# Performance work log

Hardware: AMD Instinct MI355X
Metric: run time of the kernel (lower is better)

Reference implementation:

```python
import jax, jax.numpy as jnp
import numpy as np

B, N, D, H, F = 16, 257, 1024, 16, 4096
HD = D // H
EPS = 1e-5
GATING_TEMP = 0.25  # gating_hyperparam for steep_sigmoid
SCALE = HD ** -0.5


def layer_norm(x, g, b):
    mu = jnp.mean(x, axis=-1, keepdims=True)
    var = jnp.mean(jnp.square(x - mu), axis=-1, keepdims=True)
    return (x - mu) * jax.lax.rsqrt(var + EPS) * g + b


def quick_gelu(x):
    return x * jax.nn.sigmoid(1.702 * x)


def setup_inputs() -> dict:
    key = jax.random.key(0)
    ks = jax.random.split(key, 24)
    s = 0.02
    inp = {
        'hidden_states': jax.random.normal(ks[0], (B, N, D), jnp.float32),
        'cached_hidden': jax.random.normal(ks[1], (B, N, D), jnp.float32),
        'cached_q': jax.random.normal(ks[2], (B, N, D), jnp.float32),
        'cached_k': jax.random.normal(ks[3], (B, N, D), jnp.float32),
        'cached_v': jax.random.normal(ks[4], (B, N, D), jnp.float32),
        'ln1_g': jnp.ones((D,), jnp.float32),
        'ln1_b': jnp.zeros((D,), jnp.float32),
        'wq': jax.random.normal(ks[5], (D, D), jnp.float32) * s,
        'bq': jnp.zeros((D,), jnp.float32),
        'wk': jax.random.normal(ks[6], (D, D), jnp.float32) * s,
        'bk': jnp.zeros((D,), jnp.float32),
        'wv': jax.random.normal(ks[7], (D, D), jnp.float32) * s,
        'bv': jnp.zeros((D,), jnp.float32),
        'wo': jax.random.normal(ks[8], (D, D), jnp.float32) * s,
        'bo': jnp.zeros((D,), jnp.float32),
        'ln2_g': jnp.ones((D,), jnp.float32),
        'ln2_b': jnp.zeros((D,), jnp.float32),
        'w1': jax.random.normal(ks[9], (D, F), jnp.float32) * s,
        'b1': jnp.zeros((F,), jnp.float32),
        'w2': jax.random.normal(ks[10], (F, D), jnp.float32) * s,
        'b2': jnp.zeros((D,), jnp.float32),
        'threshold': jnp.float32(0.5),
    }
    return inp


def reference(hidden_states, cached_hidden, cached_q, cached_k, cached_v,
              ln1_g, ln1_b, wq, bq, wk, bk, wv, bv, wo, bo,
              ln2_g, ln2_b, w1, b1, w2, b2, threshold):
    # layer_norm1 + QKV projection (layer_norm1_qkv_projection)
    h_ln = layer_norm(hidden_states, ln1_g, ln1_b)
    q = h_ln @ wq + bq
    k = h_ln @ wk + bk
    v = h_ln @ wv + bv

    # reuse module: cosine^1 similarity vs cached hidden, steep_sigmoid gating
    # against learned threshold; soft gather/scatter blend of cached states.
    num = jnp.sum(cached_hidden * hidden_states, axis=-1)           # [B,N]
    den = (jnp.linalg.norm(cached_hidden, axis=-1)
           * jnp.linalg.norm(hidden_states, axis=-1) + 1e-8)
    sim = num / den                                                 # [B,N]
    gate = jax.nn.sigmoid((sim - threshold) / GATING_TEMP)[..., None]  # [B,N,1]

    hidden = gate * cached_hidden + (1.0 - gate) * hidden_states
    q = gate * cached_q + (1.0 - gate) * q
    k = gate * cached_k + (1.0 - gate) * k
    v = gate * cached_v + (1.0 - gate) * v

    # manual bmm-softmax-bmm attention
    qh = (q * SCALE).reshape(B, N, H, HD).transpose(0, 2, 1, 3)  # [B,H,N,hd]
    kh = k.reshape(B, N, H, HD).transpose(0, 2, 1, 3)
    vh = v.reshape(B, N, H, HD).transpose(0, 2, 1, 3)
    scores = jnp.einsum('bhqd,bhkd->bhqk', qh, kh)
    probs = jax.nn.softmax(scores, axis=-1)
    attn = jnp.einsum('bhqk,bhkd->bhqd', probs, vh)
    attn = attn.transpose(0, 2, 1, 3).reshape(B, N, D)
    attn = attn @ wo + bo

    hidden = hidden + attn
    residual = hidden
    hidden = layer_norm(hidden, ln2_g, ln2_b)
    hidden = quick_gelu(hidden @ w1 + b1) @ w2 + b2
    return residual + hidden
```

## Files before the change

### kernel.cpp

```cpp
#include <hip/hip_runtime.h>
#include <hip/hip_bf16.h>
#include <stdint.h>

#define BB   16
#define SEQ  257
#define DD   1024
#define NH   16
#define HD_  64
#define FF   4096
#define MM   (BB*SEQ)
#define MPAD2 4352
#define SPAD 272
#define VPAD 288
#define SCALE_Q 0.125f

typedef __bf16 bf16x8 __attribute__((ext_vector_type(8)));
typedef float  f32x4  __attribute__((ext_vector_type(4)));
typedef unsigned short u16;

__device__ __forceinline__ u16 f2bf(float f) {
  uint32_t u = __float_as_uint(f);
  uint32_t r = (u + 0x7FFFu + ((u >> 16) & 1u)) >> 16;
  return (u16)r;
}
__device__ __forceinline__ float bf2f(u16 u) {
  return __uint_as_float(((uint32_t)u) << 16);
}
__device__ __forceinline__ void gll16(const void* g, void* l) {
  __builtin_amdgcn_global_load_lds(
      (const __attribute__((address_space(1))) void*)g,
      (__attribute__((address_space(3))) void*)l, 16, 0, 0);
}
__device__ __forceinline__ float wsum(float v) {
  #pragma unroll
  for (int o = 1; o < 64; o <<= 1) v += __shfl_xor(v, o);
  return v;
}

__global__ __launch_bounds__(256) void transpose_kernel(
    const float* __restrict__ in, u16* __restrict__ out, int R, int C) {
  __shared__ float tile[64][65];
  int ctiles = C >> 6;
  int r0 = (blockIdx.x / ctiles) << 6, c0 = (blockIdx.x % ctiles) << 6;
  int tx = threadIdx.x & 63, ty = threadIdx.x >> 6;
  #pragma unroll
  for (int it = 0; it < 16; ++it) {
    int rr = it * 4 + ty;
    tile[rr][tx] = in[(size_t)(r0 + rr) * C + c0 + tx];
  }
  __syncthreads();
  #pragma unroll
  for (int it = 0; it < 16; ++it) {
    int rr = it * 4 + ty;
    out[(size_t)(c0 + rr) * R + r0 + tx] = f2bf(tile[tx][rr]);
  }
}

__global__ __launch_bounds__(256) void vtrans_kernel(
    const u16* __restrict__ vb, u16* __restrict__ vt) {
  __shared__ u16 tile[64][72];
  const int bh = blockIdx.x, c = blockIdx.y;
  const int tx = threadIdx.x & 63, ty = threadIdx.x >> 6;
  const u16* src = vb + (size_t)bh * SPAD * HD_;
  u16* dst = vt + (size_t)bh * HD_ * VPAD;
  #pragma unroll
  for (int it = 0; it < 16; ++it) {
    int r = it * 4 + ty;
    int nn = c * 64 + r;  int nnc = nn < SPAD ? nn : SPAD - 1;
    tile[r][tx] = src[(size_t)nnc * HD_ + tx];
  }
  __syncthreads();
  #pragma unroll
  for (int it = 0; it < 16; ++it) {
    int hd = it * 4 + ty;
    int col = c * 64 + tx;
    if (col < VPAD) dst[(size_t)hd * VPAD + col] = tile[tx][hd];
  }
}

__global__ __launch_bounds__(256) void ln1_gate_kernel(
    const float* __restrict__ h, const float* __restrict__ c,
    const float* __restrict__ g, const float* __restrict__ bta,
    const float* __restrict__ thr, u16* __restrict__ hln,
    float* __restrict__ hblend, float* __restrict__ gate) {
  int m = blockIdx.x, t = threadIdx.x, l = t & 63, w = t >> 6;
  const float4 hv = *(const float4*)(h + (size_t)m * DD + t * 4);
  const float4 cv = *(const float4*)(c + (size_t)m * DD + t * 4);
  float sh = hv.x + hv.y + hv.z + hv.w;
  float sh2 = hv.x*hv.x + hv.y*hv.y + hv.z*hv.z + hv.w*hv.w;
  float sch = hv.x*cv.x + hv.y*cv.y + hv.z*cv.z + hv.w*cv.w;
  float sc2 = cv.x*cv.x + cv.y*cv.y + cv.z*cv.z + cv.w*cv.w;
  sh = wsum(sh); sh2 = wsum(sh2); sch = wsum(sch); sc2 = wsum(sc2);
  __shared__ float red[4][4];
  if (l == 0) { red[w][0]=sh; red[w][1]=sh2; red[w][2]=sch; red[w][3]=sc2; }
  __syncthreads();
  float Sh  = red[0][0]+red[1][0]+red[2][0]+red[3][0];
  float Sh2 = red[0][1]+red[1][1]+red[2][1]+red[3][1];
  float Sch = red[0][2]+red[1][2]+red[2][2]+red[3][2];
  float Sc2 = red[0][3]+red[1][3]+red[2][3]+red[3][3];
  float mean = Sh * (1.f/DD);
  float var  = Sh2 * (1.f/DD) - mean*mean;
  float rs   = rsqrtf(var + 1e-5f);
  float sim  = Sch / (sqrtf(Sc2)*sqrtf(Sh2) + 1e-8f);
  float gv   = 1.f / (1.f + __expf(-(sim - thr[0]) * 4.0f));
  float4 gg = *(const float4*)(g + t*4);
  float4 bb = *(const float4*)(bta + t*4);
  ushort4 ob;
  ob.x = f2bf((hv.x-mean)*rs*gg.x + bb.x);
  ob.y = f2bf((hv.y-mean)*rs*gg.y + bb.y);
  ob.z = f2bf((hv.z-mean)*rs*gg.z + bb.z);
  ob.w = f2bf((hv.w-mean)*rs*gg.w + bb.w);
  *(ushort4*)(hln + (size_t)m * DD + t * 4) = ob;
  float4 hb;
  hb.x = gv*cv.x + (1.f-gv)*hv.x;  hb.y = gv*cv.y + (1.f-gv)*hv.y;
  hb.z = gv*cv.z + (1.f-gv)*hv.z;  hb.w = gv*cv.w + (1.f-gv)*hv.w;
  *(float4*)(hblend + (size_t)m * DD + t * 4) = hb;
  if (t == 0) gate[m] = gv;
}

__global__ __launch_bounds__(256) void ln2_kernel(
    const float* __restrict__ in, const float* __restrict__ g,
    const float* __restrict__ bta, u16* __restrict__ outb) {
  int m = blockIdx.x, t = threadIdx.x, l = t & 63, w = t >> 6;
  const float4 hv = *(const float4*)(in + (size_t)m * DD + t * 4);
  float sh = hv.x + hv.y + hv.z + hv.w;
  float sh2 = hv.x*hv.x + hv.y*hv.y + hv.z*hv.z + hv.w*hv.w;
  sh = wsum(sh); sh2 = wsum(sh2);
  __shared__ float red[4][2];
  if (l == 0) { red[w][0] = sh; red[w][1] = sh2; }
  __syncthreads();
  float Sh  = red[0][0]+red[1][0]+red[2][0]+red[3][0];
  float Sh2 = red[0][1]+red[1][1]+red[2][1]+red[3][1];
  float mean = Sh * (1.f/DD);
  float rs = rsqrtf(Sh2 * (1.f/DD) - mean*mean + 1e-5f);
  float4 gg = *(const float4*)(g + t*4);
  float4 bb = *(const float4*)(bta + t*4);
  ushort4 ob;
  ob.x = f2bf((hv.x-mean)*rs*gg.x + bb.x);
  ob.y = f2bf((hv.y-mean)*rs*gg.y + bb.y);
  ob.z = f2bf((hv.z-mean)*rs*gg.z + bb.z);
  ob.w = f2bf((hv.w-mean)*rs*gg.w + bb.w);
  *(ushort4*)(outb + (size_t)m * DD + t * 4) = ob;
}

#define VMW4 do { asm volatile("s_waitcnt vmcnt(4)" ::: "memory"); \
                  __builtin_amdgcn_sched_barrier(0); } while(0)
#define VMW0 do { asm volatile("s_waitcnt vmcnt(0)" ::: "memory"); \
                  __builtin_amdgcn_sched_barrier(0); } while(0)

#define STG_A(T_, KS_, SLOT_) do { \
  const u16* _g = pA + (T_)*64 + (KS_)*32; \
  gll16(_g, &sA[SLOT_][KS_][0] + tid*8); \
  gll16(_g + rowStep, &sA[SLOT_][KS_][0] + 4096 + tid*8); } while(0)
#define STG_B(T_, KS_, SLOT_) do { \
  const u16* _g = pB + (T_)*64 + (KS_)*32; \
  gll16(_g, &sB[SLOT_][KS_][0] + tid*8); \
  gll16(_g + rowStep, &sB[SLOT_][KS_][0] + 4096 + tid*8); } while(0)

#define PHASE(SLOT_, KS_, MH_, RB_, STG_STMT, VM_STMT) do { \
  { const u16* _pa = &sA[SLOT_][KS_][aBase + (MH_)*2048]; \
    av[0] = *(const bf16x8*)(_pa);      av[1] = *(const bf16x8*)(_pa+512); \
    av[2] = *(const bf16x8*)(_pa+1024); av[3] = *(const bf16x8*)(_pa+1536); } \
  if (RB_) { const u16* _pb = &sB[SLOT_][KS_][bBase]; \
    fv[0] = *(const bf16x8*)(_pb);      fv[1] = *(const bf16x8*)(_pb+512); \
    fv[2] = *(const bf16x8*)(_pb+1024); fv[3] = *(const bf16x8*)(_pb+1536); } \
  STG_STMT; \
  __builtin_amdgcn_s_barrier(); \
  asm volatile("s_waitcnt lgkmcnt(0)" ::: "memory"); \
  __builtin_amdgcn_sched_barrier(0); \
  __builtin_amdgcn_s_setprio(1); \
  _Pragma("unroll") \
  for (int f = 0; f < 4; ++f) \
    _Pragma("unroll") \
    for (int n = 0; n < 4; ++n) \
      acc[(MH_)*4+f][n] = __builtin_amdgcn_mfma_f32_16x16x32_bf16( \
          av[f], fv[n], acc[(MH_)*4+f][n], 0, 0, 0); \
  __builtin_amdgcn_s_setprio(0); \
  VM_STMT; \
  __builtin_amdgcn_s_barrier(); } while(0)

template<int EPI, int KT>
__global__ __launch_bounds__(512, 2) void gemm256(
    const u16* __restrict__ A, const u16* __restrict__ Bt,
    int Kstride, int kBase0,
    const float* __restrict__ bias,
    const float* __restrict__ gate,
    const float* __restrict__ c0, const float* __restrict__ c1, const float* __restrict__ c2,
    const float* __restrict__ bq, const float* __restrict__ bk, const float* __restrict__ bvp,
    u16* __restrict__ qb, u16* __restrict__ kb, u16* __restrict__ vb,
    u16* __restrict__ outb, u16* __restrict__ partb) {
  const int tid = threadIdx.x, w = tid >> 6, l = tid & 63, lr = l & 15, lh = l >> 4;
  const int wm = w >> 2, wn = w & 3;
  const int n0 = blockIdx.x * 256, m0 = blockIdx.y * 256;
  const int kBase = kBase0 + blockIdx.z * (KT * 64);

  __shared__ u16 sA[2][2][8192];
  __shared__ u16 sB[2][2][8192];

  f32x4 acc[8][4];
  f32x4 zero = {0.f, 0.f, 0.f, 0.f};
  #pragma unroll
  for (int i = 0; i < 8; ++i)
    #pragma unroll
    for (int j = 0; j < 4; ++j) acc[i][j] = zero;

  const int rS = tid >> 2, cS = (tid & 3) * 8;
  const u16* pA = A  + (size_t)(m0 + rS) * Kstride + kBase + cS;
  const u16* pB = Bt + (size_t)(n0 + rS) * Kstride + kBase + cS;
  const size_t rowStep = (size_t)128 * Kstride;

  const int aBase = (wm*128 + lr) * 32 + lh * 8;
  const int bBase = (wn*64  + lr) * 32 + lh * 8;
  bf16x8 av[4], fv[4];

  STG_A(0,0,0);  STG_B(0,0,0);
  STG_A(0,1,0);  STG_B(0,1,0);
  STG_A(1,0,1);  STG_B(1,0,1);
  asm volatile("s_waitcnt vmcnt(4)" ::: "memory");
  __builtin_amdgcn_sched_barrier(0);
  __builtin_amdgcn_s_barrier();

  #pragma unroll 1
  for (int i = 0; i < KT/2 - 1; ++i) {
    const int jB = 2*i+1, nA = 2*i+2, nB = 2*i+3;
    PHASE(0,0,0,1, STG_A(jB,1,1), ((void)0));
    PHASE(0,0,1,0, STG_B(jB,1,1), ((void)0));
    PHASE(0,1,0,1, STG_A(nA,0,0), ((void)0));
    PHASE(0,1,1,0, STG_B(nA,0,0), VMW4);
    PHASE(1,0,0,1, STG_A(nA,1,0), ((void)0));
    PHASE(1,0,1,0, STG_B(nA,1,0), ((void)0));
    PHASE(1,1,0,1, STG_A(nB,0,1), ((void)0));
    PHASE(1,1,1,0, STG_B(nB,0,1), VMW4);
  }
  PHASE(0,0,0,1, STG_A(KT-1,1,1), ((void)0));
  PHASE(0,0,1,0, STG_B(KT-1,1,1), ((void)0));
  PHASE(0,1,0,1, ((void)0), ((void)0));
  PHASE(0,1,1,0, ((void)0), VMW0);
  PHASE(1,0,0,1, ((void)0), ((void)0));
  PHASE(1,0,1,0, ((void)0), ((void)0));
  PHASE(1,1,0,1, ((void)0), ((void)0));
  PHASE(1,1,1,0, ((void)0), ((void)0));

  const int crow = m0 + wm*128, ccol = n0 + wn*64;
  if constexpr (EPI == 0) {
    const int which = n0 >> 10;
    const float* cb = which==0 ? bq : (which==1 ? bk : bvp);
    const float* cp = which==0 ? c0 : (which==1 ? c1 : c2);
    u16* dst = which==0 ? qb : (which==1 ? kb : vb);
    const float scl = which==0 ? SCALE_Q : 1.0f;
    #pragma unroll
    for (int mi = 0; mi < 8; ++mi)
      #pragma unroll
      for (int rr = 0; rr < 4; ++rr) {
        const int row = crow + mi*16 + lh*4 + rr;
        if (row < MM) {
          const float gv = gate[row];
          const int bidx = row / SEQ, nn = row - bidx * SEQ;
          #pragma unroll
          for (int ni = 0; ni < 4; ++ni) {
            const int col = ccol + ni*16 + lr;
            const int d = col & 1023, hd = d & 63, hh = d >> 6;
            const float lin = acc[mi][ni][rr] + cb[d];
            const float val = (gv * cp[(size_t)row*DD + d] + (1.f - gv) * lin) * scl;
            dst[((size_t)(bidx*NH + hh)*SPAD + nn)*HD_ + hd] = f2bf(val);
          }
        }
      }
  } else if constexpr (EPI == 2) {
    #pragma unroll
    for (int mi = 0; mi < 8; ++mi)
      #pragma unroll
      for (int rr = 0; rr < 4; ++rr) {
        const int row = crow + mi*16 + lh*4 + rr;
        if (row < MM) {
          #pragma unroll
          for (int ni = 0; ni < 4; ++ni) {
            const int col = ccol + ni*16 + lr;
            const float x = acc[mi][ni][rr] + bias[col];
            const float s = 1.f / (1.f + __expf(-1.702f * x));
            outb[(size_t)row*FF + col] = f2bf(x * s);
          }
        }
      }
  } else {
    u16* pp = partb + (size_t)blockIdx.z * ((size_t)MPAD2 * 1024);
    #pragma unroll
    for (int mi = 0; mi < 8; ++mi)
      #pragma unroll
      for (int rr = 0; rr < 4; ++rr) {
        const int row = crow + mi*16 + lh*4 + rr;
        if (row < MM) {
          #pragma unroll
          for (int ni = 0; ni < 4; ++ni) {
            const int col = ccol + ni*16 + lr;
            pp[(size_t)row*1024 + col] = f2bf(acc[mi][ni][rr]);
          }
        }
      }
  }
}

__global__ __launch_bounds__(256) void reduce_mlp2(
    const u16* __restrict__ parts, const float* __restrict__ bias,
    const float* __restrict__ resid, float* __restrict__ out) {
  const size_t PS = (size_t)MPAD2 * 1024;
  const int row = blockIdx.x, t = threadIdx.x, c = t * 4;
  const size_t base = (size_t)row * 1024 + c;
  float4 r = *(const float4*)(resid + base);
  float4 b = *(const float4*)(bias + c);
  float o0 = r.x + b.x, o1 = r.y + b.y, o2 = r.z + b.z, o3 = r.w + b.w;
  #pragma unroll
  for (int p = 0; p < 4; ++p) {
    ushort4 u = *(const ushort4*)(parts + p*PS + base);
    o0 += bf2f(u.x);  o1 += bf2f(u.y);  o2 += bf2f(u.z);  o3 += bf2f(u.w);
  }
  float4 o;  o.x = o0;  o.y = o1;  o.z = o2;  o.w = o3;
  *(float4*)(out + base) = o;
}

template<int EPI>
__global__ __launch_bounds__(256) void gemm_bt(
    const u16* __restrict__ A, const u16* __restrict__ Bt, int K,
    const float* __restrict__ bias,
    const float* __restrict__ addsrc, float* __restrict__ outf) {
  const int tid = threadIdx.x, w = tid >> 6, l = tid & 63, lr = l & 15, lh = l >> 4;
  const int n0 = blockIdx.x * 128, m0 = blockIdx.y * 128;
  const int wm = w >> 1, wn = w & 1;
  __shared__ u16 sA[2][4096], sB[2][4096];
  f32x4 acc[4][4];
  f32x4 zero = {0.f, 0.f, 0.f, 0.f};
  #pragma unroll
  for (int i = 0; i < 4; ++i)
    #pragma unroll
    for (int j = 0; j < 4; ++j) acc[i][j] = zero;

  const int r0 = tid >> 2, cc = (tid & 3) * 8;
  const u16* ga0 = A  + (size_t)(m0 + r0) * K + cc;
  const u16* ga1 = A  + (size_t)(m0 + 64 + r0) * K + cc;
  const u16* gb0 = Bt + (size_t)(n0 + r0) * K + cc;
  const u16* gb1 = Bt + (size_t)(n0 + 64 + r0) * K + cc;

  const int nt = K >> 5;
  gll16(ga0, &sA[0][w*512]);  gll16(ga1, &sA[0][2048 + w*512]);
  gll16(gb0, &sB[0][w*512]);  gll16(gb1, &sB[0][2048 + w*512]);

  for (int t = 0; t < nt; ++t) {
    const int cur = t & 1;
    __syncthreads();
    if (t + 1 < nt) {
      const int k0 = (t + 1) << 5;
      gll16(ga0 + k0, &sA[cur^1][w*512]);  gll16(ga1 + k0, &sA[cur^1][2048 + w*512]);
      gll16(gb0 + k0, &sB[cur^1][w*512]);  gll16(gb1 + k0, &sB[cur^1][2048 + w*512]);
    }
    bf16x8 af[4], bfr[4];
    #pragma unroll
    for (int mi = 0; mi < 4; ++mi)
      af[mi] = *(const bf16x8*)&sA[cur][(wm*64 + mi*16 + lr)*32 + lh*8];
    #pragma unroll
    for (int ni = 0; ni < 4; ++ni)
      bfr[ni] = *(const bf16x8*)&sB[cur][(wn*64 + ni*16 + lr)*32 + lh*8];
    #pragma unroll
    for (int mi = 0; mi < 4; ++mi)
      #pragma unroll
      for (int ni = 0; ni < 4; ++ni)
        acc[mi][ni] = __builtin_amdgcn_mfma_f32_16x16x32_bf16(af[mi], bfr[ni], acc[mi][ni], 0, 0, 0);
  }

  #pragma unroll
  for (int mi = 0; mi < 4; ++mi)
    #pragma unroll
    for (int r = 0; r < 4; ++r) {
      const int row = m0 + wm*64 + mi*16 + lh*4 + r;
      if (row < MM) {
        #pragma unroll
        for (int ni = 0; ni < 4; ++ni) {
          const int col = n0 + wn*64 + ni*16 + lr;
          outf[(size_t)row*DD + col] = acc[mi][ni][r] + bias[col] + addsrc[(size_t)row*DD + col];
        }
      }
    }
}

__global__ __launch_bounds__(256) void attn_kernel(
    const u16* __restrict__ qb, const u16* __restrict__ kb,
    const u16* __restrict__ vt, u16* __restrict__ attn_out) {
  __shared__ u16 P[64 * 296];
  const int bh = blockIdx.x, b = bh >> 4, hh = bh & 15;
  const int q0 = blockIdx.y * 64;
  const int tid = threadIdx.x, w = tid >> 6, l = tid & 63, lr = l & 15, lh = l >> 4;
  const u16* qp = qb + (size_t)bh * SPAD * HD_;
  const u16* kp = kb + (size_t)bh * SPAD * HD_;
  const u16* vp = vt + (size_t)bh * HD_ * VPAD;

  const int qr = q0 + w*16 + lr;
  const int qrc = qr < 271 ? qr : 271;
  bf16x8 aq0 = *(const bf16x8*)(qp + (size_t)qrc*HD_ + lh*8);
  bf16x8 aq1 = *(const bf16x8*)(qp + (size_t)qrc*HD_ + 32 + lh*8);

  f32x4 st[18];
  f32x4 zero = {0.f,0.f,0.f,0.f};
  #pragma unroll
  for (int t = 0; t < 18; ++t) st[t] = zero;
  #pragma unroll
  for (int t = 0; t < 18; ++t) {
    int key = t*16 + lr;  int keyc = key < 271 ? key : 271;
    bf16x8 b0 = *(const bf16x8*)(kp + (size_t)keyc*HD_ + lh*8);
    bf16x8 b1 = *(const bf16x8*)(kp + (size_t)keyc*HD_ + 32 + lh*8);
    st[t] = __builtin_amdgcn_mfma_f32_16x16x32_bf16(aq0, b0, st[t], 0, 0, 0);
    st[t] = __builtin_amdgcn_mfma_f32_16x16x32_bf16(aq1, b1, st[t], 0, 0, 0);
  }
  #pragma unroll
  for (int t = 0; t < 18; ++t) {
    int key = t*16 + lr;
    if (key >= SEQ) { st[t][0]=-1e30f; st[t][1]=-1e30f; st[t][2]=-1e30f; st[t][3]=-1e30f; }
  }
  float mr[4], sr[4];
  #pragma unroll
  for (int r = 0; r < 4; ++r) {
    float m = st[0][r];
    #pragma unroll
    for (int t = 1; t < 18; ++t) m = fmaxf(m, st[t][r]);
    m = fmaxf(m, __shfl_xor(m, 1));  m = fmaxf(m, __shfl_xor(m, 2));
    m = fmaxf(m, __shfl_xor(m, 4));  m = fmaxf(m, __shfl_xor(m, 8));
    mr[r] = m;  sr[r] = 0.f;
  }
  #pragma unroll
  for (int t = 0; t < 18; ++t)
    #pragma unroll
    for (int r = 0; r < 4; ++r) {
      float p = __expf(st[t][r] - mr[r]);
      st[t][r] = p;  sr[r] += p;
    }
  #pragma unroll
  for (int r = 0; r < 4; ++r) {
    sr[r] += __shfl_xor(sr[r], 1);  sr[r] += __shfl_xor(sr[r], 2);
    sr[r] += __shfl_xor(sr[r], 4);  sr[r] += __shfl_xor(sr[r], 8);
  }
  #pragma unroll
  for (int t = 0; t < 18; ++t)
    #pragma unroll
    for (int r = 0; r < 4; ++r)
      P[(w*16 + lh*4 + r)*296 + t*16 + lr] = f2bf(st[t][r]);
  __syncthreads();

  f32x4 o[4];
  #pragma unroll
  for (int ni = 0; ni < 4; ++ni) o[ni] = zero;
  #pragma unroll
  for (int ks = 0; ks < 9; ++ks) {
    bf16x8 pa = *(const bf16x8*)&P[(w*16 + lr)*296 + ks*32 + lh*8];
    #pragma unroll
    for (int ni = 0; ni < 4; ++ni) {
      bf16x8 bv_ = *(const bf16x8*)(vp + (size_t)(ni*16 + lr)*VPAD + ks*32 + lh*8);
      o[ni] = __builtin_amdgcn_mfma_f32_16x16x32_bf16(pa, bv_, o[ni], 0, 0, 0);
    }
  }
  #pragma unroll
  for (int r = 0; r < 4; ++r) {
    const int qrow = q0 + w*16 + lh*4 + r;
    if (qrow < SEQ) {
      const float inv = 1.f / sr[r];
      #pragma unroll
      for (int ni = 0; ni < 4; ++ni)
        attn_out[(size_t)(b*SEQ + qrow)*DD + hh*HD_ + ni*16 + lr] = f2bf(o[ni][r] * inv);
    }
  }
}

extern "C" void kernel_launch(void* const* d_in, const int* in_sizes, int n_in,
                              void* d_out, int out_size, void* d_ws, size_t ws_size,
                              hipStream_t stream) {
  (void)in_sizes; (void)n_in; (void)out_size; (void)ws_size;
  const float* hidden   = (const float*)d_in[0];
  const float* cached_h = (const float*)d_in[1];
  const float* cached_q = (const float*)d_in[2];
  const float* cached_k = (const float*)d_in[3];
  const float* cached_v = (const float*)d_in[4];
  const float* ln1_g = (const float*)d_in[5];
  const float* ln1_b = (const float*)d_in[6];
  const float* wq = (const float*)d_in[7];
  const float* bq = (const float*)d_in[8];
  const float* wk = (const float*)d_in[9];
  const float* bk = (const float*)d_in[10];
  const float* wv = (const float*)d_in[11];
  const float* bv = (const float*)d_in[12];
  const float* wo = (const float*)d_in[13];
  const float* bo = (const float*)d_in[14];
  const float* ln2_g = (const float*)d_in[15];
  const float* ln2_b = (const float*)d_in[16];
  const float* w1 = (const float*)d_in[17];
  const float* b1 = (const float*)d_in[18];
  const float* w2 = (const float*)d_in[19];
  const float* b2 = (const float*)d_in[20];
  const float* thr = (const float*)d_in[21];
  float* out = (float*)d_out;

  char* ws = (char*)d_ws;
  size_t off = 0;
  auto alloc = [&](size_t bytes) {
    void* p = ws + off;  off += (bytes + 255) & ~(size_t)255;  return p;
  };
  u16*   wqkvT  = (u16*)alloc(3072ull * 1024 * 2);
  u16*   woT    = (u16*)alloc(1024ull * 1024 * 2);
  u16*   w1T    = (u16*)alloc(4096ull * 1024 * 2);
  u16*   w2T    = (u16*)alloc(1024ull * 4096 * 2);
  float* gate   = (float*)alloc((size_t)MPAD2 * 4);
  float* resid2 = (float*)alloc((size_t)MPAD2 * DD * 4);
  u16*   regA   = (u16*)alloc((size_t)MPAD2 * DD * 2);
  u16 *hln = regA, *attn_o = regA, *ln2out = regA;
  const size_t QKV_B  = (size_t)256 * SPAD * HD_ * 2;
  const size_t VT_B   = (size_t)256 * HD_ * VPAD * 2;
  const size_t PART_B = (size_t)MPAD2 * 1024 * 2;
  const size_t partsOff = 3*QKV_B + VT_B;
  char*  regB   = (char*)alloc(partsOff + 4*PART_B);
  u16*   qbuf   = (u16*)regB;
  u16*   kbuf   = (u16*)(regB + QKV_B);
  u16*   vbuf   = (u16*)(regB + 2*QKV_B);
  u16*   vtb    = (u16*)(regB + 3*QKV_B);
  float* hblend = (float*)(regB + partsOff);
  u16*   mid    = (u16*)regB;
  u16*   parts  = (u16*)(regB + partsOff);

  dim3 blk(256), blk5(512);
  transpose_kernel<<<dim3(256),  blk, 0, stream>>>(wq, wqkvT,                 1024, 1024);
  transpose_kernel<<<dim3(256),  blk, 0, stream>>>(wk, wqkvT + 1024*1024,     1024, 1024);
  transpose_kernel<<<dim3(256),  blk, 0, stream>>>(wv, wqkvT + 2*1024*1024,   1024, 1024);
  transpose_kernel<<<dim3(256),  blk, 0, stream>>>(wo, woT,                   1024, 1024);
  transpose_kernel<<<dim3(1024), blk, 0, stream>>>(w1, w1T,                   1024, 4096);
  transpose_kernel<<<dim3(1024), blk, 0, stream>>>(w2, w2T,                   4096, 1024);

  ln1_gate_kernel<<<dim3(MM), blk, 0, stream>>>(hidden, cached_h, ln1_g, ln1_b, thr,
                                                hln, hblend, gate);

  gemm256<0,16><<<dim3(12, 17), blk5, 0, stream>>>(hln, wqkvT, 1024, 0,
      nullptr, gate, cached_q, cached_k, cached_v, bq, bk, bv,
      qbuf, kbuf, vbuf, nullptr, nullptr);

  vtrans_kernel<<<dim3(256, 5), blk, 0, stream>>>(vbuf, vtb);
  attn_kernel<<<dim3(256, 5), blk, 0, stream>>>(qbuf, kbuf, vtb, attn_o);

  gemm_bt<1><<<dim3(8, 33), blk, 0, stream>>>(attn_o, woT, 1024, bo, hblend, resid2);

  ln2_kernel<<<dim3(MM), blk, 0, stream>>>(resid2, ln2_g, ln2_b, ln2out);

  gemm256<2,16><<<dim3(16, 17), blk5, 0, stream>>>(ln2out, w1T, 1024, 0,
      b1, nullptr, nullptr, nullptr, nullptr, nullptr, nullptr, nullptr,
      nullptr, nullptr, nullptr, mid, nullptr);

  gemm256<3,16><<<dim3(4, 17, 4), blk5, 0, stream>>>(mid, w2T, 4096, 0,
      nullptr, nullptr, nullptr, nullptr, nullptr, nullptr, nullptr, nullptr,
      nullptr, nullptr, nullptr, nullptr, parts);

  reduce_mlp2<<<dim3(MM), blk, 0, stream>>>(parts, b2, resid2, out);
}
```

Measured before the change: 363.6 us.

## Merge weight transposes, swizzle LDS, triple-buffer and XCD-remap out-projection GEMM

```diff
diff --git a/kernel.cpp b/kernel.cpp
--- a/kernel.cpp
+++ b/kernel.cpp
@@ -37,22 +37,34 @@
   return v;
 }
 
-__global__ __launch_bounds__(256) void transpose_kernel(
-    const float* __restrict__ in, u16* __restrict__ out, int R, int C) {
+__global__ __launch_bounds__(256) void transpose_all(
+    const float* __restrict__ wq, const float* __restrict__ wk,
+    const float* __restrict__ wv, const float* __restrict__ wo,
+    const float* __restrict__ w1, const float* __restrict__ w2,
+    u16* __restrict__ wqkvT, u16* __restrict__ woT,
+    u16* __restrict__ w1T, u16* __restrict__ w2T) {
   __shared__ float tile[64][65];
-  int ctiles = C >> 6;
-  int r0 = (blockIdx.x / ctiles) << 6, c0 = (blockIdx.x % ctiles) << 6;
-  int tx = threadIdx.x & 63, ty = threadIdx.x >> 6;
+  const int bid = blockIdx.x;
+  const float* src;  u16* dst;  int R, C, b;
+  if (bid < 768)       { int s = bid >> 8;  b = bid & 255;
+                         src = s==0?wq:(s==1?wk:wv);  dst = wqkvT + s*1024*1024;
+                         R = 1024; C = 1024; }
+  else if (bid < 1024) { src = wo;  dst = woT;  b = bid - 768;   R = 1024; C = 1024; }
+  else if (bid < 2048) { src = w1;  dst = w1T;  b = bid - 1024;  R = 1024; C = 4096; }
+  else                 { src = w2;  dst = w2T;  b = bid - 2048;  R = 4096; C = 1024; }
+  const int ctiles = C >> 6;
+  const int r0 = (b / ctiles) << 6, c0 = (b % ctiles) << 6;
+  const int tx = threadIdx.x & 63, ty = threadIdx.x >> 6;
   #pragma unroll
   for (int it = 0; it < 16; ++it) {
     int rr = it * 4 + ty;
-    tile[rr][tx] = in[(size_t)(r0 + rr) * C + c0 + tx];
+    tile[rr][tx] = src[(size_t)(r0 + rr) * C + c0 + tx];
   }
   __syncthreads();
   #pragma unroll
   for (int it = 0; it < 16; ++it) {
     int rr = it * 4 + ty;
-    out[(size_t)(c0 + rr) * R + r0 + tx] = f2bf(tile[tx][rr]);
+    dst[(size_t)(c0 + rr) * R + r0 + tx] = f2bf(tile[tx][rr]);
   }
 }
 
@@ -204,13 +216,15 @@
     #pragma unroll
     for (int j = 0; j < 4; ++j) acc[i][j] = zero;
 
-  const int rS = tid >> 2, cS = (tid & 3) * 8;
+  const int rS = tid >> 2;
+  const int cS = ((tid & 3) ^ ((tid >> 3) & 3)) * 8;
   const u16* pA = A  + (size_t)(m0 + rS) * Kstride + kBase + cS;
   const u16* pB = Bt + (size_t)(n0 + rS) * Kstride + kBase + cS;
   const size_t rowStep = (size_t)128 * Kstride;
 
-  const int aBase = (wm*128 + lr) * 32 + lh * 8;
-  const int bBase = (wn*64  + lr) * 32 + lh * 8;
+  const int cx = ((lh ^ ((lr >> 1) & 3)) & 3) * 8;
+  const int aBase = (wm*128 + lr) * 32 + cx;
+  const int bBase = (wn*64  + lr) * 32 + cx;
   bf16x8 av[4], fv[4];
 
   STG_A(0,0,0);  STG_B(0,0,0);
@@ -300,33 +314,21 @@
   }
 }
 
-__global__ __launch_bounds__(256) void reduce_mlp2(
-    const u16* __restrict__ parts, const float* __restrict__ bias,
-    const float* __restrict__ resid, float* __restrict__ out) {
-  const size_t PS = (size_t)MPAD2 * 1024;
-  const int row = blockIdx.x, t = threadIdx.x, c = t * 4;
-  const size_t base = (size_t)row * 1024 + c;
-  float4 r = *(const float4*)(resid + base);
-  float4 b = *(const float4*)(bias + c);
-  float o0 = r.x + b.x, o1 = r.y + b.y, o2 = r.z + b.z, o3 = r.w + b.w;
-  #pragma unroll
-  for (int p = 0; p < 4; ++p) {
-    ushort4 u = *(const ushort4*)(parts + p*PS + base);
-    o0 += bf2f(u.x);  o1 += bf2f(u.y);  o2 += bf2f(u.z);  o3 += bf2f(u.w);
-  }
-  float4 o;  o.x = o0;  o.y = o1;  o.z = o2;  o.w = o3;
-  *(float4*)(out + base) = o;
-}
-
 template<int EPI>
-__global__ __launch_bounds__(256) void gemm_bt(
-    const u16* __restrict__ A, const u16* __restrict__ Bt, int K,
+__global__ __launch_bounds__(256, 3) void gemm_bt(
+    const u16* __restrict__ A, const u16* __restrict__ Bt,
+    int Kstride, int Kiter,
     const float* __restrict__ bias,
     const float* __restrict__ addsrc, float* __restrict__ outf) {
   const int tid = threadIdx.x, w = tid >> 6, l = tid & 63, lr = l & 15, lh = l >> 4;
-  const int n0 = blockIdx.x * 128, m0 = blockIdx.y * 128;
+  const int Mt = gridDim.x;
+  const int f = blockIdx.y * Mt + blockIdx.x;
+  const int nwg = Mt * gridDim.y;
+  const int q8 = nwg >> 3, r8 = nwg & 7, xcd = f & 7, lin = f >> 3;
+  const int swz = (xcd < r8 ? xcd * (q8 + 1) : r8 * (q8 + 1) + (xcd - r8) * q8) + lin;
+  const int m0 = (swz % Mt) * 128, n0 = (swz / Mt) * 128;
   const int wm = w >> 1, wn = w & 1;
-  __shared__ u16 sA[2][4096], sB[2][4096];
+  __shared__ u16 sA[3][4096], sB[3][4096];
   f32x4 acc[4][4];
   f32x4 zero = {0.f, 0.f, 0.f, 0.f};
   #pragma unroll
@@ -334,37 +336,57 @@
     #pragma unroll
     for (int j = 0; j < 4; ++j) acc[i][j] = zero;
 
-  const int r0 = tid >> 2, cc = (tid & 3) * 8;
-  const u16* ga0 = A  + (size_t)(m0 + r0) * K + cc;
-  const u16* ga1 = A  + (size_t)(m0 + 64 + r0) * K + cc;
-  const u16* gb0 = Bt + (size_t)(n0 + r0) * K + cc;
-  const u16* gb1 = Bt + (size_t)(n0 + 64 + r0) * K + cc;
-
-  const int nt = K >> 5;
-  gll16(ga0, &sA[0][w*512]);  gll16(ga1, &sA[0][2048 + w*512]);
-  gll16(gb0, &sB[0][w*512]);  gll16(gb1, &sB[0][2048 + w*512]);
-
+  const int rS = tid >> 2;
+  const int srcC = (((tid & 3) ^ ((tid >> 3) & 3)) * 8);
+  const u16* gA = A  + (size_t)(m0 + rS) * Kstride + srcC;
+  const u16* gB = Bt + (size_t)(n0 + rS) * Kstride + srcC;
+  const size_t rStep = (size_t)64 * Kstride;
+
+  const int sL = (lr >> 1) & 3;
+  const int coff = ((lh ^ sL) & 3) * 8;
+  const int rdA = (wm*64 + lr) * 32 + coff;
+  const int rdB = (wn*64 + lr) * 32 + coff;
+
+  #define STAGE(S_, T_) do { \
+    const int _ko = (T_) << 5; \
+    gll16(gA + _ko,         &sA[S_][0]    + tid*8); \
+    gll16(gA + _ko + rStep, &sA[S_][2048] + tid*8); \
+    gll16(gB + _ko,         &sB[S_][0]    + tid*8); \
+    gll16(gB + _ko + rStep, &sB[S_][2048] + tid*8); \
+  } while(0)
+
+  const int nt = Kiter >> 5;
+  STAGE(0, 0);
+  STAGE(1, 1);
+  #pragma unroll 1
   for (int t = 0; t < nt; ++t) {
-    const int cur = t & 1;
-    __syncthreads();
-    if (t + 1 < nt) {
-      const int k0 = (t + 1) << 5;
-      gll16(ga0 + k0, &sA[cur^1][w*512]);  gll16(ga1 + k0, &sA[cur^1][2048 + w*512]);
-      gll16(gb0 + k0, &sB[cur^1][w*512]);  gll16(gb1 + k0, &sB[cur^1][2048 + w*512]);
+    const int sc = t % 3;
+    __builtin_amdgcn_s_barrier();
+    if (t + 2 < nt) {
+      STAGE((t + 2) % 3, t + 2);
+      asm volatile("s_waitcnt vmcnt(8)" ::: "memory");
+    } else if (t + 1 < nt) {
+      asm volatile("s_waitcnt vmcnt(4)" ::: "memory");
+    } else {
+      asm volatile("s_waitcnt vmcnt(0)" ::: "memory");
     }
+    __builtin_amdgcn_sched_barrier(0);
+    __builtin_amdgcn_s_barrier();
+    __builtin_amdgcn_sched_barrier(0);
     bf16x8 af[4], bfr[4];
     #pragma unroll
     for (int mi = 0; mi < 4; ++mi)
-      af[mi] = *(const bf16x8*)&sA[cur][(wm*64 + mi*16 + lr)*32 + lh*8];
+      af[mi] = *(const bf16x8*)&sA[sc][rdA + mi*512];
     #pragma unroll
     for (int ni = 0; ni < 4; ++ni)
-      bfr[ni] = *(const bf16x8*)&sB[cur][(wn*64 + ni*16 + lr)*32 + lh*8];
+      bfr[ni] = *(const bf16x8*)&sB[sc][rdB + ni*512];
     #pragma unroll
     for (int mi = 0; mi < 4; ++mi)
       #pragma unroll
       for (int ni = 0; ni < 4; ++ni)
         acc[mi][ni] = __builtin_amdgcn_mfma_f32_16x16x32_bf16(af[mi], bfr[ni], acc[mi][ni], 0, 0, 0);
   }
+  #undef STAGE
 
   #pragma unroll
   for (int mi = 0; mi < 4; ++mi)
@@ -379,6 +401,24 @@
         }
       }
     }
+}
+
+__global__ __launch_bounds__(256) void reduce_mlp2(
+    const u16* __restrict__ parts, const float* __restrict__ bias,
+    const float* __restrict__ resid, float* __restrict__ out) {
+  const size_t PS = (size_t)MPAD2 * 1024;
+  const int row = blockIdx.x, t = threadIdx.x, c = t * 4;
+  const size_t base = (size_t)row * 1024 + c;
+  float4 r = *(const float4*)(resid + base);
+  float4 b = *(const float4*)(bias + c);
+  float o0 = r.x + b.x, o1 = r.y + b.y, o2 = r.z + b.z, o3 = r.w + b.w;
+  #pragma unroll
+  for (int p = 0; p < 4; ++p) {
+    ushort4 u = *(const ushort4*)(parts + p*PS + base);
+    o0 += bf2f(u.x);  o1 += bf2f(u.y);  o2 += bf2f(u.z);  o3 += bf2f(u.w);
+  }
+  float4 o;  o.x = o0;  o.y = o1;  o.z = o2;  o.w = o3;
+  *(float4*)(out + base) = o;
 }
 
 __global__ __launch_bounds__(256) void attn_kernel(
@@ -522,12 +562,8 @@
   u16*   parts  = (u16*)(regB + partsOff);
 
   dim3 blk(256), blk5(512);
-  transpose_kernel<<<dim3(256),  blk, 0, stream>>>(wq, wqkvT,                 1024, 1024);
-  transpose_kernel<<<dim3(256),  blk, 0, stream>>>(wk, wqkvT + 1024*1024,     1024, 1024);
-  transpose_kernel<<<dim3(256),  blk, 0, stream>>>(wv, wqkvT + 2*1024*1024,   1024, 1024);
-  transpose_kernel<<<dim3(256),  blk, 0, stream>>>(wo, woT,                   1024, 1024);
-  transpose_kernel<<<dim3(1024), blk, 0, stream>>>(w1, w1T,                   1024, 4096);
-  transpose_kernel<<<dim3(1024), blk, 0, stream>>>(w2, w2T,                   4096, 1024);
+  transpose_all<<<dim3(3072), blk, 0, stream>>>(wq, wk, wv, wo, w1, w2,
+                                                wqkvT, woT, w1T, w2T);
 
   ln1_gate_kernel<<<dim3(MM), blk, 0, stream>>>(hidden, cached_h, ln1_g, ln1_b, thr,
                                                 hln, hblend, gate);
@@ -539,7 +575,8 @@
   vtrans_kernel<<<dim3(256, 5), blk, 0, stream>>>(vbuf, vtb);
   attn_kernel<<<dim3(256, 5), blk, 0, stream>>>(qbuf, kbuf, vtb, attn_o);
 
-  gemm_bt<1><<<dim3(8, 33), blk, 0, stream>>>(attn_o, woT, 1024, bo, hblend, resid2);
+  gemm_bt<1><<<dim3(33, 8), blk, 0, stream>>>(attn_o, woT, 1024, 1024, bo,
+      hblend, resid2);
 
   ln2_kernel<<<dim3(MM), blk, 0, stream>>>(resid2, ln2_g, ln2_b, ln2out);
 
```

After: 341.0 us. 6.2% less time.
